# Optimization experiments

Measured on AMD Instinct MI355X. Metric: run time of the kernel, lower is better.

The kernel has to match this reference:

```python
import jax, jax.numpy as jnp
import numpy as np

B, L, D, N, V = 32, 4096, 128, 5, 128  # batch, seq, embed dim, n-gram order, alphabet size


def setup_inputs() -> dict:
    key = jax.random.key(0)
    k1, k2, k3 = jax.random.split(key, 3)
    x = jax.random.randint(k1, (B, L), 0, V, dtype=jnp.int32)
    emb = jax.random.normal(k2, (V, D), dtype=jnp.float32)
    W = jax.random.normal(k3, (V, D * (N - 1)), dtype=jnp.float32) * 0.05
    b = jnp.zeros((V,), dtype=jnp.float32)
    return {"x": x, "emb": emb, "W": W, "b": b}


def reference(x, emb, W, b):
    n1 = N - 1  # context window size
    x_enc = emb[x]  # (B, L, D) embedding gather
    # enc[:, j, k*D:(k+1)*D] = x_enc[:, j - n1 + k] for j >= n1; zeros for j < n1.
    # Build each slot by right-shifting the embedded sequence by (n1 - k).
    Lcur = x.shape[1]
    parts = [jnp.pad(x_enc, ((0, 0), (n1 - k, 0), (0, 0)))[:, :Lcur] for k in range(n1)]
    enc = jnp.concatenate(parts, axis=-1)  # (B, L, n1*D)
    valid = (jnp.arange(Lcur) >= n1)[None, :, None]
    enc = jnp.where(valid, enc, jnp.zeros((), enc.dtype))
    # linear: logits = enc @ W^T + b  -> (B, L, V)
    logits = jnp.einsum("blf,vf->blv", enc, W) + b
    return logits
```

## Files before the change

### kernel.cpp

```cpp
#include <hip/hip_runtime.h>

constexpr int Bn = 32;
constexpr int Ln = 4096;
constexpr int Dn = 128;
constexpr int Vn = 128;
constexpr int N1 = 4;

typedef float vfloat4 __attribute__((ext_vector_type(4)));

__global__ void build_table_kernel(const float* __restrict__ emb,
                                   const float* __restrict__ W,
                                   const float* __restrict__ bias,
                                   float* __restrict__ T) {
    const int kt = blockIdx.x;
    const int k  = kt >> 7;
    const int t  = kt & 127;
    const int v  = threadIdx.x;

    __shared__ float4 e[Dn / 4];
    if (threadIdx.x < Dn / 4) {
        e[threadIdx.x] = ((const float4*)(emb + t * Dn))[threadIdx.x];
    }
    __syncthreads();

    const float4* w = (const float4*)(W + (size_t)v * (Dn * N1) + k * Dn);
    float acc = (k == 0) ? bias[v] : 0.f;
#pragma unroll
    for (int i = 0; i < Dn / 4; ++i) {
        float4 wv = w[i];
        float4 ev = e[i];
        acc += wv.x * ev.x + wv.y * ev.y + wv.z * ev.z + wv.w * ev.w;
    }
    T[(size_t)kt * Vn + v] = acc;
}

__global__ void __launch_bounds__(256, 4)
ngram_logits_kernel(const int* __restrict__ x,
                    const float* __restrict__ T,
                    const float* __restrict__ bias,
                    float* __restrict__ out) {
    const int tid = blockIdx.x * 256 + threadIdx.x;
    const int vq  = tid & 31;
    const int G   = tid >> 5;
    const int basepos = G << 3;
    const int j0      = basepos & (Ln - 1);

    const vfloat4* Tq   = (const vfloat4*)T;
    vfloat4*       outq = (vfloat4*)out;
    vfloat4*       ob   = outq + (size_t)basepos * 32 + vq;

    int w[11];
    const int4 xb = *(const int4*)(x + basepos);
    const int4 xc = *(const int4*)(x + basepos + 4);
    w[4] = xb.x; w[5] = xb.y; w[6] = xb.z; w[7] = xb.w;
    w[8] = xc.x; w[9] = xc.y; w[10] = xc.z;

    if (j0 == 0) {
        const vfloat4 bv = ((const vfloat4*)bias)[vq];
#pragma unroll
        for (int i = 0; i < 4; ++i)
            __builtin_nontemporal_store(bv, ob + i * 32);
    } else {
        const int4 xa = *(const int4*)(x + basepos - 4);
        w[0] = xa.x; w[1] = xa.y; w[2] = xa.z; w[3] = xa.w;
        vfloat4 a0 = Tq[(size_t)(0 * Vn + w[0]) * 32 + vq];
        vfloat4 a1 = Tq[(size_t)(0 * Vn + w[1]) * 32 + vq];
        vfloat4 a2 = Tq[(size_t)(0 * Vn + w[2]) * 32 + vq];
        vfloat4 a3 = Tq[(size_t)(0 * Vn + w[3]) * 32 + vq];
#pragma unroll
        for (int k = 1; k < N1; ++k) {
            a0 += Tq[(size_t)(k * Vn + w[0 + k]) * 32 + vq];
            a1 += Tq[(size_t)(k * Vn + w[1 + k]) * 32 + vq];
            a2 += Tq[(size_t)(k * Vn + w[2 + k]) * 32 + vq];
            a3 += Tq[(size_t)(k * Vn + w[3 + k]) * 32 + vq];
        }
        __builtin_nontemporal_store(a0, ob + 0 * 32);
        __builtin_nontemporal_store(a1, ob + 1 * 32);
        __builtin_nontemporal_store(a2, ob + 2 * 32);
        __builtin_nontemporal_store(a3, ob + 3 * 32);
    }

    {
        vfloat4 a0 = Tq[(size_t)(0 * Vn + w[4]) * 32 + vq];
        vfloat4 a1 = Tq[(size_t)(0 * Vn + w[5]) * 32 + vq];
        vfloat4 a2 = Tq[(size_t)(0 * Vn + w[6]) * 32 + vq];
        vfloat4 a3 = Tq[(size_t)(0 * Vn + w[7]) * 32 + vq];
#pragma unroll
        for (int k = 1; k < N1; ++k) {
            a0 += Tq[(size_t)(k * Vn + w[4 + k]) * 32 + vq];
            a1 += Tq[(size_t)(k * Vn + w[5 + k]) * 32 + vq];
            a2 += Tq[(size_t)(k * Vn + w[6 + k]) * 32 + vq];
            a3 += Tq[(size_t)(k * Vn + w[7 + k]) * 32 + vq];
        }
        __builtin_nontemporal_store(a0, ob + 4 * 32);
        __builtin_nontemporal_store(a1, ob + 5 * 32);
        __builtin_nontemporal_store(a2, ob + 6 * 32);
        __builtin_nontemporal_store(a3, ob + 7 * 32);
    }
}

extern "C" void kernel_launch(void* const* d_in, const int* in_sizes, int n_in,
                              void* d_out, int out_size, void* d_ws, size_t ws_size,
                              hipStream_t stream) {
    const int*   x    = (const int*)d_in[0];
    const float* emb  = (const float*)d_in[1];
    const float* W    = (const float*)d_in[2];
    const float* bias = (const float*)d_in[3];
    float*       out  = (float*)d_out;
    float*       T    = (float*)d_ws;

    build_table_kernel<<<N1 * Vn, Vn, 0, stream>>>(emb, W, bias, T);

    ngram_logits_kernel<<<2048, 256, 0, stream>>>(x, T, bias, out);
}
```

Before: 91.92 us.

## Precompute pairwise-summed n-gram tables to halve gathers per output

Adds a kernel that builds a 128x128 pair table for context slots (0,1) and (2,3), each entry the sum of two per-slot projected rows. The main kernel then does two gathers per position instead of four. This trades fewer L2-resident gathers for a 16MB extra table write and larger-footprint random reads. It falls back to the direct path when the workspace is too small.

```diff
diff --git a/kernel.cpp b/kernel.cpp
--- a/kernel.cpp
+++ b/kernel.cpp
@@ -34,11 +34,87 @@
     T[(size_t)kt * Vn + v] = acc;
 }
 
+__global__ void __launch_bounds__(256, 8)
+pair_build_kernel(const float* __restrict__ T, float* __restrict__ P) {
+    const int fid  = blockIdx.x * 256 + threadIdx.x;
+    const int half = fid >> 19;
+    const int rem  = fid & ((1 << 19) - 1);
+    const int ab   = rem >> 5;
+    const int vq   = rem & 31;
+    const int a    = ab >> 7;
+    const int b    = ab & 127;
+
+    const vfloat4* Ta = (const vfloat4*)(T + (size_t)((half * 2 + 0) * Vn + a) * Vn);
+    const vfloat4* Tb = (const vfloat4*)(T + (size_t)((half * 2 + 1) * Vn + b) * Vn);
+    const vfloat4  s  = Ta[vq] + Tb[vq];
+    __builtin_nontemporal_store(s, (vfloat4*)P + (size_t)fid);
+}
+
 __global__ void __launch_bounds__(256, 4)
-ngram_logits_kernel(const int* __restrict__ x,
-                    const float* __restrict__ T,
-                    const float* __restrict__ bias,
-                    float* __restrict__ out) {
+ngram_logits_pair_kernel(const int* __restrict__ x,
+                         const float* __restrict__ P,
+                         const float* __restrict__ bias,
+                         float* __restrict__ out) {
+    const int tid = blockIdx.x * 256 + threadIdx.x;
+    const int vq  = tid & 31;
+    const int G   = tid >> 5;
+    const int basepos = G << 3;
+    const int j0      = basepos & (Ln - 1);
+
+    const vfloat4* P01 = (const vfloat4*)P;
+    const vfloat4* P23 = (const vfloat4*)(P + (size_t)Vn * Vn * Vn);
+    vfloat4*      outq = (vfloat4*)out;
+    vfloat4*      ob   = outq + (size_t)basepos * 32 + vq;
+
+    int w[11];
+    const int4 xb = *(const int4*)(x + basepos);
+    const int4 xc = *(const int4*)(x + basepos + 4);
+    w[4] = xb.x; w[5] = xb.y; w[6] = xb.z; w[7] = xb.w;
+    w[8] = xc.x; w[9] = xc.y; w[10] = xc.z;
+
+    if (j0 == 0) {
+        const vfloat4 bv = ((const vfloat4*)bias)[vq];
+#pragma unroll
+        for (int i = 0; i < 4; ++i)
+            __builtin_nontemporal_store(bv, ob + i * 32);
+    } else {
+        const int4 xa = *(const int4*)(x + basepos - 4);
+        w[0] = xa.x; w[1] = xa.y; w[2] = xa.z; w[3] = xa.w;
+        vfloat4 a0 = P01[(size_t)((w[0] << 7) + w[1]) * 32 + vq];
+        vfloat4 a1 = P01[(size_t)((w[1] << 7) + w[2]) * 32 + vq];
+        vfloat4 a2 = P01[(size_t)((w[2] << 7) + w[3]) * 32 + vq];
+        vfloat4 a3 = P01[(size_t)((w[3] << 7) + w[4]) * 32 + vq];
+        a0 += P23[(size_t)((w[2] << 7) + w[3]) * 32 + vq];
+        a1 += P23[(size_t)((w[3] << 7) + w[4]) * 32 + vq];
+        a2 += P23[(size_t)((w[4] << 7) + w[5]) * 32 + vq];
+        a3 += P23[(size_t)((w[5] << 7) + w[6]) * 32 + vq];
+        __builtin_nontemporal_store(a0, ob + 0 * 32);
+        __builtin_nontemporal_store(a1, ob + 1 * 32);
+        __builtin_nontemporal_store(a2, ob + 2 * 32);
+        __builtin_nontemporal_store(a3, ob + 3 * 32);
+    }
+
+    {
+        vfloat4 a0 = P01[(size_t)((w[4] << 7) + w[5]) * 32 + vq];
+        vfloat4 a1 = P01[(size_t)((w[5] << 7) + w[6]) * 32 + vq];
+        vfloat4 a2 = P01[(size_t)((w[6] << 7) + w[7]) * 32 + vq];
+        vfloat4 a3 = P01[(size_t)((w[7] << 7) + w[8]) * 32 + vq];
+        a0 += P23[(size_t)((w[6] << 7) + w[7]) * 32 + vq];
+        a1 += P23[(size_t)((w[7] << 7) + w[8]) * 32 + vq];
+        a2 += P23[(size_t)((w[8] << 7) + w[9]) * 32 + vq];
+        a3 += P23[(size_t)((w[9] << 7) + w[10]) * 32 + vq];
+        __builtin_nontemporal_store(a0, ob + 4 * 32);
+        __builtin_nontemporal_store(a1, ob + 5 * 32);
+        __builtin_nontemporal_store(a2, ob + 6 * 32);
+        __builtin_nontemporal_store(a3, ob + 7 * 32);
+    }
+}
+
+__global__ void __launch_bounds__(256, 4)
+ngram_logits_direct_kernel(const int* __restrict__ x,
+                           const float* __restrict__ T,
+                           const float* __restrict__ bias,
+                           float* __restrict__ out) {
     const int tid = blockIdx.x * 256 + threadIdx.x;
     const int vq  = tid & 31;
     const int G   = tid >> 5;
@@ -107,9 +183,16 @@
     const float* W    = (const float*)d_in[2];
     const float* bias = (const float*)d_in[3];
     float*       out  = (float*)d_out;
-    float*       T    = (float*)d_ws;
 
+    float* T = (float*)d_ws;
     build_table_kernel<<<N1 * Vn, Vn, 0, stream>>>(emb, W, bias, T);
 
-    ngram_logits_kernel<<<2048, 256, 0, stream>>>(x, T, bias, out);
+    const size_t need = (size_t)(N1 * Vn * Vn) * 4 + (size_t)2 * Vn * Vn * Vn * 4;
+    if (ws_size >= need) {
+        float* P = T + (size_t)N1 * Vn * Vn;
+        pair_build_kernel<<<4096, 256, 0, stream>>>(T, P);
+        ngram_logits_pair_kernel<<<2048, 256, 0, stream>>>(x, P, bias, out);
+    } else {
+        ngram_logits_direct_kernel<<<2048, 256, 0, stream>>>(x, T, bias, out);
+    }
 }
```

New measurement: 112.5 us. 1.22x slower.
